# Kernel optimization log

Measured on AMD Instinct MI355X. Metric: run time of the kernel, lower is better.

The kernel has to match this reference:

```python
import jax, jax.numpy as jnp
import numpy as np

B, T, D, DIM = 32, 2048, 1024, 1024


def setup_inputs() -> dict:
    key = jax.random.key(0)
    ks = jax.random.split(key, 7)
    def glorot(k, shape):
        lim = np.sqrt(6.0 / (shape[0] + shape[1]))
        return jax.random.uniform(k, shape, jnp.float32, -lim, lim)
    return {
        "input_states": jax.random.normal(ks[0], (B, T, D), jnp.float32),
        "last_state": jax.random.normal(ks[1], (B, D), jnp.float32),
        "Wy": glorot(ks[2], (D, DIM)),
        "Wh": glorot(ks[3], (D, DIM)),
        "w": glorot(ks[4], (DIM, 1)),
        "Wp": glorot(ks[5], (D, DIM)),
        "Wx": glorot(ks[6], (D, DIM)),
    }


def reference(input_states, last_state, Wy, Wh, w, Wp, Wx):
    # hs: (B,T,dim); last_state projection broadcast over T (the original
    # tiles last_state via a ones-matmul; a plain broadcast is the same math)
    hs = jnp.einsum("btd,de->bte", input_states, Wy)
    hproj = last_state @ Wh                      # (B,dim)
    m = jax.nn.relu(hs + hproj[:, None, :])      # (B,T,dim)
    scores = jnp.einsum("bte,eo->bt", m, w[:, :1])  # squeeze last dim
    alpha = jax.nn.softmax(scores, axis=-1)      # (B,T)
    r = jnp.einsum("bt,btd->bd", alpha, input_states)
    out = jax.nn.relu(r @ Wp + last_state @ Wx)  # (B,dim)
    return out
```

## Files before the change

### kernel.cpp

```cpp
#include <hip/hip_runtime.h>
#include <hip/hip_bf16.h>
#include <stdint.h>

#define BB 32
#define TT 2048
#define DD 1024
#define DIMQ 1024
#define MTOT (BB*TT)

typedef __attribute__((ext_vector_type(8))) __bf16 bf16x8;
typedef __attribute__((ext_vector_type(4))) float f32x4;

__device__ __forceinline__ unsigned short f2bf(float f) {
    unsigned int u = __float_as_uint(f);
    u += 0x7FFF + ((u >> 16) & 1);
    return (unsigned short)(u >> 16);
}
__device__ __forceinline__ float bf2f(unsigned short s) {
    return __uint_as_float(((unsigned int)s) << 16);
}

__device__ __forceinline__ void load_lds16(const void* g, void* l) {
    __builtin_amdgcn_global_load_lds(
        (const __attribute__((address_space(1))) unsigned int*)g,
        (__attribute__((address_space(3))) unsigned int*)l,
        16, 0, 0);
}

__global__ void cast_x(const float* __restrict__ x, unsigned short* __restrict__ xb) {
    long i = ((long)blockIdx.x * blockDim.x + threadIdx.x) * 4;
    float4 a = *(const float4*)(x + i);
    ushort4 o;
    o.x = f2bf(a.x); o.y = f2bf(a.y); o.z = f2bf(a.z); o.w = f2bf(a.w);
    *(ushort4*)(xb + i) = o;
}

__global__ void transpose_cast(const float* __restrict__ Wsrc, unsigned short* __restrict__ Wdst) {
    __shared__ float tile[32][33];
    int bx = blockIdx.x * 32;
    int by = blockIdx.y * 32;
    int tx = threadIdx.x & 31;
    int ty4 = (threadIdx.x >> 5) * 4;
    #pragma unroll
    for (int r = 0; r < 4; r++)
        tile[ty4 + r][tx] = Wsrc[(size_t)(by + ty4 + r) * DIMQ + bx + tx];
    __syncthreads();
    #pragma unroll
    for (int r = 0; r < 4; r++)
        Wdst[(size_t)(bx + ty4 + r) * DD + by + tx] = f2bf(tile[tx][ty4 + r]);
}

__global__ void vecmat2(const float* __restrict__ last,
                        const float* __restrict__ Wh, const float* __restrict__ Wx,
                        float* __restrict__ hproj, float* __restrict__ lsWx) {
    __shared__ float vs[DD];
    __shared__ float red[4][64];
    int b = blockIdx.y;
    int e0 = blockIdx.x * 64;
    const float* Mat = blockIdx.z ? Wx : Wh;
    float* outp = blockIdx.z ? lsWx : hproj;
    int tid = threadIdx.x;
    for (int d = tid; d < DD; d += 256) vs[d] = last[b * DD + d];
    __syncthreads();
    int e = tid & 63, dg = tid >> 6;
    int d0 = dg * 256;
    const float* Mp = Mat + (size_t)d0 * DIMQ + e0 + e;
    float acc = 0.f;
    #pragma unroll 8
    for (int d = 0; d < 256; d++) acc += vs[d0 + d] * Mp[(size_t)d * DIMQ];
    red[dg][e] = acc;
    __syncthreads();
    if (dg == 0)
        outp[b * DIMQ + e0 + e] = red[0][e] + red[1][e] + red[2][e] + red[3][e];
}

__global__ __launch_bounds__(256, 2)
void gemm_scores(const unsigned short* __restrict__ Xb,
                 const unsigned short* __restrict__ WyT,
                 const float* __restrict__ hproj,
                 const float* __restrict__ wvec,
                 float* __restrict__ partials) {
    __shared__ unsigned short Alds[4096];
    __shared__ unsigned short Blds[8192];
    __shared__ float lp[128];

    int x = blockIdx.x;
    int mtile = x >> 2, ntile = x & 3;
    int tid = threadIdx.x;
    int lane = tid & 63;
    int wave = tid >> 6;

    if (tid < 128) lp[tid] = 0.f;

    const int rowA0 = mtile * 128;
    const int colB0 = ntile * 256;

    int rsel = lane & 15;
    int koff = (lane >> 4) * 8;
    int s0 = tid >> 6;

    const unsigned short* Ag0 = Xb  + (size_t)(rowA0 + s0 * 16 + rsel) * DD + koff;
    const unsigned short* Ag1 = Ag0 + (size_t)64 * DD;
    const unsigned short* Bg0 = WyT + (size_t)(colB0 + s0 * 16 + rsel) * DD + koff;
    const unsigned short* Bg1 = Bg0 + (size_t)64 * DD;
    const unsigned short* Bg2 = Bg0 + (size_t)128 * DD;
    const unsigned short* Bg3 = Bg0 + (size_t)192 * DD;

    unsigned short* Al0 = &Alds[tid * 8];
    unsigned short* Al1 = &Alds[(tid + 256) * 8];
    unsigned short* Bl0 = &Blds[tid * 8];
    unsigned short* Bl1 = &Blds[(tid + 256) * 8];
    unsigned short* Bl2 = &Blds[(tid + 512) * 8];
    unsigned short* Bl3 = &Blds[(tid + 768) * 8];

    int wr = wave >> 1;
    int wc = wave & 1;

    f32x4 acc[4][8] = {};

    for (int kk = 0; kk < DD; kk += 32) {
        load_lds16(Ag0 + kk, Al0);
        load_lds16(Ag1 + kk, Al1);
        load_lds16(Bg0 + kk, Bl0);
        load_lds16(Bg1 + kk, Bl1);
        load_lds16(Bg2 + kk, Bl2);
        load_lds16(Bg3 + kk, Bl3);
        __syncthreads();

        bf16x8 af[4], bfr[8];
        #pragma unroll
        for (int i = 0; i < 4; i++)
            af[i] = *reinterpret_cast<const bf16x8*>(&Alds[((wr * 4 + i) * 64 + lane) * 8]);
        #pragma unroll
        for (int j = 0; j < 8; j++)
            bfr[j] = *reinterpret_cast<const bf16x8*>(&Blds[((wc * 8 + j) * 64 + lane) * 8]);
        #pragma unroll
        for (int i = 0; i < 4; i++)
            #pragma unroll
            for (int j = 0; j < 8; j++)
                acc[i][j] = __builtin_amdgcn_mfma_f32_16x16x32_bf16(af[i], bfr[j], acc[i][j], 0, 0, 0);
        __syncthreads();
    }

    int b = rowA0 / TT;
    int q = lane >> 4, l15 = lane & 15;

    float hpv[8], wvv[8];
    #pragma unroll
    for (int j = 0; j < 8; j++) {
        int n = colB0 + wc * 128 + j * 16 + l15;
        hpv[j] = hproj[b * DIMQ + n];
        wvv[j] = wvec[n];
    }

    #pragma unroll
    for (int i = 0; i < 4; i++) {
        f32x4 s = {0.f, 0.f, 0.f, 0.f};
        #pragma unroll
        for (int j = 0; j < 8; j++) {
            #pragma unroll
            for (int r = 0; r < 4; r++) {
                float v = acc[i][j][r] + hpv[j];
                v = v > 0.f ? v : 0.f;
                s[r] += v * wvv[j];
            }
        }
        #pragma unroll
        for (int off = 1; off < 16; off <<= 1) {
            s[0] += __shfl_xor(s[0], off);
            s[1] += __shfl_xor(s[1], off);
            s[2] += __shfl_xor(s[2], off);
            s[3] += __shfl_xor(s[3], off);
        }
        if (l15 == 0) {
            int mrow = wr * 64 + i * 16 + q * 4;
            atomicAdd(&lp[mrow + 0], s[0]);
            atomicAdd(&lp[mrow + 1], s[1]);
            atomicAdd(&lp[mrow + 2], s[2]);
            atomicAdd(&lp[mrow + 3], s[3]);
        }
    }
    __syncthreads();
    if (tid < 128)
        partials[(size_t)ntile * MTOT + rowA0 + tid] = lp[tid];
}

__global__ void softmax_alpha(const float* __restrict__ partials, float* __restrict__ alpha) {
    __shared__ float wred[4];
    __shared__ float wsum[4];
    int b = blockIdx.x;
    int tid = threadIdx.x;
    float s[8];
    float mx = -1e30f;
    #pragma unroll
    for (int c = 0; c < 8; c++) {
        int t = b * TT + tid + c * 256;
        float v = 0.f;
        #pragma unroll
        for (int p = 0; p < 4; p++) v += partials[(size_t)p * MTOT + t];
        s[c] = v;
        mx = fmaxf(mx, v);
    }
    for (int off = 32; off; off >>= 1) mx = fmaxf(mx, __shfl_xor(mx, off));
    if ((tid & 63) == 0) wred[tid >> 6] = mx;
    __syncthreads();
    mx = fmaxf(fmaxf(wred[0], wred[1]), fmaxf(wred[2], wred[3]));
    float sum = 0.f;
    #pragma unroll
    for (int c = 0; c < 8; c++) { s[c] = expf(s[c] - mx); sum += s[c]; }
    for (int off = 32; off; off >>= 1) sum += __shfl_xor(sum, off);
    if ((tid & 63) == 0) wsum[tid >> 6] = sum;
    __syncthreads();
    sum = wsum[0] + wsum[1] + wsum[2] + wsum[3];
    float inv = 1.f / sum;
    #pragma unroll
    for (int c = 0; c < 8; c++) alpha[b * TT + tid + c * 256] = s[c] * inv;
}

__global__ void weighted_sum(const unsigned short* __restrict__ Xb,
                             const float* __restrict__ alpha,
                             float* __restrict__ r_part) {
    __shared__ float al[128];
    int tc = blockIdx.x, b = blockIdx.y, tid = threadIdx.x;
    if (tid < 128) al[tid] = alpha[b * TT + tc * 128 + tid];
    __syncthreads();
    int d0 = tid * 4;
    const unsigned short* base = Xb + ((size_t)(b * TT + tc * 128)) * DD + d0;
    f32x4 acc = {0.f, 0.f, 0.f, 0.f};
    #pragma unroll 2
    for (int t = 0; t < 128; t++) {
        ushort4 xv = *(const ushort4*)(base + (size_t)t * DD);
        float a_ = al[t];
        acc[0] += a_ * bf2f(xv.x);
        acc[1] += a_ * bf2f(xv.y);
        acc[2] += a_ * bf2f(xv.z);
        acc[3] += a_ * bf2f(xv.w);
    }
    float* o = r_part + ((size_t)tc * BB + b) * DD + d0;
    *(float4*)o = *(float4*)&acc;
}

__global__ void final_out(const float* __restrict__ r_part, const float* __restrict__ Wp,
                          const float* __restrict__ lsWx, float* __restrict__ out) {
    __shared__ float rs[DD];
    __shared__ float red[4][64];
    int b = blockIdx.y;
    int e0 = blockIdx.x * 64;
    int tid = threadIdx.x;
    for (int d = tid; d < DD; d += 256) {
        float v = 0.f;
        #pragma unroll
        for (int p = 0; p < 16; p++) v += r_part[((size_t)p * BB + b) * DD + d];
        rs[d] = v;
    }
    __syncthreads();
    int e = tid & 63, dg = tid >> 6;
    int d0 = dg * 256;
    const float* Mp = Wp + (size_t)d0 * DIMQ + e0 + e;
    float acc = 0.f;
    #pragma unroll 8
    for (int d = 0; d < 256; d++) acc += rs[d0 + d] * Mp[(size_t)d * DIMQ];
    red[dg][e] = acc;
    __syncthreads();
    if (dg == 0) {
        float v = red[0][e] + red[1][e] + red[2][e] + red[3][e]
                + lsWx[b * DIMQ + e0 + e];
        out[b * DIMQ + e0 + e] = fmaxf(v, 0.f);
    }
}

extern "C" void kernel_launch(void* const* d_in, const int* in_sizes, int n_in,
                              void* d_out, int out_size, void* d_ws, size_t ws_size,
                              hipStream_t stream) {
    const float* x    = (const float*)d_in[0];
    const float* last = (const float*)d_in[1];
    const float* Wy   = (const float*)d_in[2];
    const float* Wh   = (const float*)d_in[3];
    const float* w    = (const float*)d_in[4];
    const float* Wp   = (const float*)d_in[5];
    const float* Wx   = (const float*)d_in[6];
    float* out = (float*)d_out;

    char* ws = (char*)d_ws;
    unsigned short* Xb   = (unsigned short*)(ws);
    unsigned short* WyT  = (unsigned short*)(ws + 134217728);
    float* hproj         = (float*)(ws + 136314880);
    float* lsWx          = (float*)(ws + 136445952);
    float* partials      = (float*)(ws + 136577024);
    float* alpha         = (float*)(ws + 137625600);
    float* r_part        = (float*)(ws + 137887744);

    cast_x<<<BB*TT*DD/4/256, 256, 0, stream>>>(x, Xb);
    transpose_cast<<<dim3(32, 32), 256, 0, stream>>>(Wy, WyT);
    vecmat2<<<dim3(DIMQ/64, BB, 2), 256, 0, stream>>>(last, Wh, Wx, hproj, lsWx);
    gemm_scores<<<512 * 4, 256, 0, stream>>>(Xb, WyT, hproj, w, partials);
    softmax_alpha<<<BB, 256, 0, stream>>>(partials, alpha);
    weighted_sum<<<dim3(TT/128, BB), 256, 0, stream>>>(Xb, alpha, r_part);
    final_out<<<dim3(DIMQ/64, BB), 256, 0, stream>>>(r_part, Wp, lsWx, out);
}
```

Before: 643.6 us.

## Double-buffer LDS tiles in scores GEMM to overlap loads with MFMA

The A and B LDS tiles become ping-pong buffers. The global-to-LDS loads for the next K step are issued right after the barrier, while MFMAs run on the current buffer, and the trailing barrier is removed so there is one sync per step. This hides global load latency behind MFMA compute. The cost is doubled LDS use per block, which could limit occupancy if other shared arrays grow.

```diff
diff --git a/kernel.cpp b/kernel.cpp
--- a/kernel.cpp
+++ b/kernel.cpp
@@ -80,8 +80,8 @@
                  const float* __restrict__ hproj,
                  const float* __restrict__ wvec,
                  float* __restrict__ partials) {
-    __shared__ unsigned short Alds[4096];
-    __shared__ unsigned short Blds[8192];
+    __shared__ unsigned short Alds[2][4096];
+    __shared__ unsigned short Blds[2][8192];
     __shared__ float lp[128];
 
     int x = blockIdx.x;
@@ -106,40 +106,45 @@
     const unsigned short* Bg2 = Bg0 + (size_t)128 * DD;
     const unsigned short* Bg3 = Bg0 + (size_t)192 * DD;
 
-    unsigned short* Al0 = &Alds[tid * 8];
-    unsigned short* Al1 = &Alds[(tid + 256) * 8];
-    unsigned short* Bl0 = &Blds[tid * 8];
-    unsigned short* Bl1 = &Blds[(tid + 256) * 8];
-    unsigned short* Bl2 = &Blds[(tid + 512) * 8];
-    unsigned short* Bl3 = &Blds[(tid + 768) * 8];
-
     int wr = wave >> 1;
     int wc = wave & 1;
 
     f32x4 acc[4][8] = {};
 
-    for (int kk = 0; kk < DD; kk += 32) {
-        load_lds16(Ag0 + kk, Al0);
-        load_lds16(Ag1 + kk, Al1);
-        load_lds16(Bg0 + kk, Bl0);
-        load_lds16(Bg1 + kk, Bl1);
-        load_lds16(Bg2 + kk, Bl2);
-        load_lds16(Bg3 + kk, Bl3);
+    load_lds16(Ag0, &Alds[0][tid * 8]);
+    load_lds16(Ag1, &Alds[0][(tid + 256) * 8]);
+    load_lds16(Bg0, &Blds[0][tid * 8]);
+    load_lds16(Bg1, &Blds[0][(tid + 256) * 8]);
+    load_lds16(Bg2, &Blds[0][(tid + 512) * 8]);
+    load_lds16(Bg3, &Blds[0][(tid + 768) * 8]);
+
+    #pragma unroll 2
+    for (int it = 0; it < 32; it++) {
+        int cur = it & 1, nxt = cur ^ 1;
         __syncthreads();
 
+        if (it < 31) {
+            int k = (it + 1) * 32;
+            load_lds16(Ag0 + k, &Alds[nxt][tid * 8]);
+            load_lds16(Ag1 + k, &Alds[nxt][(tid + 256) * 8]);
+            load_lds16(Bg0 + k, &Blds[nxt][tid * 8]);
+            load_lds16(Bg1 + k, &Blds[nxt][(tid + 256) * 8]);
+            load_lds16(Bg2 + k, &Blds[nxt][(tid + 512) * 8]);
+            load_lds16(Bg3 + k, &Blds[nxt][(tid + 768) * 8]);
+        }
+
         bf16x8 af[4], bfr[8];
         #pragma unroll
         for (int i = 0; i < 4; i++)
-            af[i] = *reinterpret_cast<const bf16x8*>(&Alds[((wr * 4 + i) * 64 + lane) * 8]);
+            af[i] = *reinterpret_cast<const bf16x8*>(&Alds[cur][((wr * 4 + i) * 64 + lane) * 8]);
         #pragma unroll
         for (int j = 0; j < 8; j++)
-            bfr[j] = *reinterpret_cast<const bf16x8*>(&Blds[((wc * 8 + j) * 64 + lane) * 8]);
+            bfr[j] = *reinterpret_cast<const bf16x8*>(&Blds[cur][((wc * 8 + j) * 64 + lane) * 8]);
         #pragma unroll
         for (int i = 0; i < 4; i++)
             #pragma unroll
             for (int j = 0; j < 8; j++)
                 acc[i][j] = __builtin_amdgcn_mfma_f32_16x16x32_bf16(af[i], bfr[j], acc[i][j], 0, 0, 0);
-        __syncthreads();
     }
 
     int b = rowA0 / TT;
```

New measurement: 658.2 us. 1.02x slower.
